# Optimization experiments

Hardware: AMD Instinct MI355X
Metric: run time of the kernel (lower is better)

## Reference

```python
import jax, jax.numpy as jnp
import numpy as np

B, T, E = 64, 512, 128
NODES, PATHS, OUT = 100000, 200000, 1000
PAD = 1  # padding_idx for node embedding


def setup_inputs() -> dict:
    key = jax.random.key(0)
    ks = jax.random.split(key, 10)
    starts = jax.random.randint(ks[0], (B, T), 0, NODES)
    paths = jax.random.randint(ks[1], (B, T), 0, PATHS)
    ends = jax.random.randint(ks[2], (B, T), 0, NODES)
    length = jax.random.randint(ks[3], (B,), 0, T)
    node_emb = jax.random.normal(ks[4], (NODES, E), dtype=jnp.float32)
    path_emb = jax.random.normal(ks[5], (PATHS, E), dtype=jnp.float32)
    W = jax.random.normal(ks[6], (E, 3 * E), dtype=jnp.float32)
    a = jax.random.normal(ks[7], (E,), dtype=jnp.float32)
    out_W = jax.random.normal(ks[8], (OUT, E), dtype=jnp.float32) * (1.0 / np.sqrt(E))
    out_b = jax.random.normal(ks[9], (OUT,), dtype=jnp.float32) * 0.01
    return dict(starts=starts, paths=paths, ends=ends, length=length,
                node_emb=node_emb, path_emb=path_emb, W=W, a=a,
                out_W=out_W, out_b=out_b)


def reference(starts, paths, ends, length, node_emb, path_emb, W, a, out_W, out_b):
    # padding_idx=1 -> that embedding row is zero
    node_emb = node_emb.at[PAD].set(0.0)
    es = node_emb[starts]          # [B,T,E]
    ep = path_emb[paths]           # [B,T,E]
    ee = node_emb[ends]            # [B,T,E]
    c = jnp.concatenate([es, ep, ee], axis=2)          # [B,T,3E]
    # dropout is identity in eval mode
    x = jnp.tanh(jnp.einsum('ed,btd->bte', W, c))      # [B,T,E]
    z = jax.nn.softmax(x @ a, axis=1)                  # [B,T] softmax over full T
    # original code sums only first length[i] attention weights (no renorm)
    mask = (jnp.arange(T)[None, :] < length[:, None]).astype(x.dtype)  # [B,T]
    v = jnp.einsum('bte,bt->be', x, z * mask)          # [B,E]
    return v @ out_W.T + out_b                          # [B,OUT]
```

## Files before the change

### kernel.cpp

```cpp
#include <hip/hip_runtime.h>

#define BB     64
#define TT     512
#define EE     128
#define NROWS  (BB * TT)
#define PADIDX 1
#define OUTN   1000

typedef __attribute__((ext_vector_type(8)))  short short8;
typedef __attribute__((ext_vector_type(16))) float f32x16;

__device__ __forceinline__ float tanh_fast(float v) {
    return 1.0f - 2.0f / (__expf(2.0f * v) + 1.0f);
}

__device__ __forceinline__ void split8(float4 a0, float4 a1, short8& hi, short8& lo) {
    float f[8] = {a0.x, a0.y, a0.z, a0.w, a1.x, a1.y, a1.z, a1.w};
#pragma unroll
    for (int i = 0; i < 8; ++i) {
        unsigned u = __float_as_uint(f[i]);
        unsigned r = (u + (0x7fffu + ((u >> 16) & 1u))) & 0xffff0000u;
        hi[i] = (short)(r >> 16);
        lo[i] = (short)(__float_as_uint(f[i] - __uint_as_float(r)) >> 16);
    }
}

__global__ __launch_bounds__(256)
void k_prep(const float* __restrict__ W, unsigned short* __restrict__ Whg,
            unsigned short* __restrict__ Wlg)
{
    const int id = blockIdx.x * 256 + threadIdx.x;
    const int j  = id & 7;
    const int l  = (id >> 3) & 63;
    const int r2 = id >> 9;
    const int ks = r2 % 24;
    const int et = r2 / 24;
    const int e  = et * 32 + (l & 31);
    const int k  = ks * 16 + (l >> 5) * 8 + j;

    const float v = W[e * 384 + k];
    unsigned u = __float_as_uint(v);
    unsigned r = (u + (0x7fffu + ((u >> 16) & 1u))) & 0xffff0000u;
    Whg[id] = (unsigned short)(r >> 16);
    Wlg[id] = (unsigned short)(__float_as_uint(v - __uint_as_float(r)) >> 16);
}

__global__ __launch_bounds__(256, 2)
void k_gemm_x(const int* __restrict__ starts, const int* __restrict__ paths,
              const int* __restrict__ ends,
              const float* __restrict__ node_emb, const float* __restrict__ path_emb,
              const unsigned short* __restrict__ Whg, const unsigned short* __restrict__ Wlg,
              const float* __restrict__ a, float* __restrict__ x, float* __restrict__ s)
{
    __shared__ float mrg[64 * 128];

    const int tid  = threadIdx.x;
    const int lane = tid & 63;
    const int w    = tid >> 6;
    const int mg   = w >> 1;
    const int kg   = w & 1;
    const int fr   = lane & 31;
    const int kh   = lane >> 5;
    const int r0   = blockIdx.x * 64;

    const int row = r0 + mg * 32 + fr;
    const int i0 = starts[row], i1 = paths[row], i2 = ends[row];
    const char* baseA0 = (const char*)node_emb + (size_t)i0 * 512 + kh * 32;
    const char* baseA1 = (const char*)path_emb + (size_t)i1 * 512 + kh * 32;
    const char* baseA2 = (const char*)node_emb + (size_t)i2 * 512 + kh * 32;
    const bool pad0 = (i0 == PADIDX), pad2 = (i2 == PADIDX);

    const char* pbh = (const char*)Whg + lane * 16;
    const char* pbl = (const char*)Wlg + lane * 16;

    f32x16 acc[4];
#pragma unroll
    for (int ni = 0; ni < 4; ++ni)
#pragma unroll
        for (int i = 0; i < 16; ++i) acc[ni][i] = 0.0f;

    float4 a0b[2], a1b[2];
    short8 bhb[2][4], blb[2][4];

#define ISSUE_A(SLOT, KS) do {                                                  \
    const int seg_ = (KS) >> 3;                                                 \
    const char* p_ = (seg_ == 0 ? baseA0 : (seg_ == 1 ? baseA1 : baseA2))       \
                   + ((KS) & 7) * 64;                                           \
    a0b[SLOT] = *(const float4*)p_;                                             \
    a1b[SLOT] = *(const float4*)(p_ + 16);                                      \
} while (0)

#define ISSUE_B(SLOT, KS) do {                                                  \
    _Pragma("unroll")                                                           \
    for (int ni_ = 0; ni_ < 4; ++ni_) {                                         \
        bhb[SLOT][ni_] = *(const short8*)(pbh + ni_ * 24576 + (KS) * 1024);     \
        blb[SLOT][ni_] = *(const short8*)(pbl + ni_ * 24576 + (KS) * 1024);     \
    }                                                                           \
} while (0)

#define KLOOP(KS0) do {                                                         \
    ISSUE_A(0, (KS0));  ISSUE_A(1, (KS0) + 1);  ISSUE_B(0, (KS0));              \
    _Pragma("unroll")                                                           \
    for (int j = 0; j < 12; ++j) {                                              \
        const int seg_c = ((KS0) + j) >> 3;                                     \
        float4 ca0 = a0b[j & 1], ca1 = a1b[j & 1];                              \
        const bool pad_ = (seg_c == 0) ? pad0 : ((seg_c == 2) ? pad2 : false);  \
        if (pad_) { ca0 = make_float4(0.f, 0.f, 0.f, 0.f); ca1 = ca0; }         \
        if (j + 2 < 12) ISSUE_A(j & 1, (KS0) + j + 2);                          \
        if (j + 1 < 12) ISSUE_B((j + 1) & 1, (KS0) + j + 1);                    \
        short8 ah, al;                                                          \
        split8(ca0, ca1, ah, al);                                               \
        _Pragma("unroll")                                                       \
        for (int ni = 0; ni < 4; ++ni) {                                        \
            acc[ni] = __builtin_amdgcn_mfma_f32_32x32x16_bf16(ah, bhb[j & 1][ni], acc[ni], 0, 0, 0); \
            acc[ni] = __builtin_amdgcn_mfma_f32_32x32x16_bf16(ah, blb[j & 1][ni], acc[ni], 0, 0, 0); \
            acc[ni] = __builtin_amdgcn_mfma_f32_32x32x16_bf16(al, bhb[j & 1][ni], acc[ni], 0, 0, 0); \
        }                                                                       \
    }                                                                           \
} while (0)

    if (kg == 0) KLOOP(0); else KLOOP(12);

#undef ISSUE_A
#undef ISSUE_B
#undef KLOOP

    if (kg == 1) {
#pragma unroll
        for (int ni = 0; ni < 4; ++ni)
#pragma unroll
            for (int r = 0; r < 16; ++r)
                mrg[(ni * 16 + r) * 128 + mg * 64 + lane] = acc[ni][r];
    }
    __syncthreads();

    if (kg == 0) {
#pragma unroll
        for (int ni = 0; ni < 4; ++ni)
#pragma unroll
            for (int r = 0; r < 16; ++r)
                acc[ni][r] += mrg[(ni * 16 + r) * 128 + mg * 64 + lane];

        float av[4];
#pragma unroll
        for (int ni = 0; ni < 4; ++ni) av[ni] = a[ni * 32 + fr];

        float sp[16];
#pragma unroll
        for (int r = 0; r < 16; ++r) sp[r] = 0.0f;

#pragma unroll
        for (int ni = 0; ni < 4; ++ni)
#pragma unroll
            for (int r = 0; r < 16; ++r) {
                const int rowl = (r & 3) + 8 * (r >> 2) + 4 * kh;
                const float tv = tanh_fast(acc[ni][r]);
                x[(size_t)(r0 + mg * 32 + rowl) * EE + ni * 32 + fr] = tv;
                sp[r] = fmaf(tv, av[ni], sp[r]);
            }

#pragma unroll
        for (int m = 1; m < 32; m <<= 1)
#pragma unroll
            for (int r = 0; r < 16; ++r) sp[r] += __shfl_xor(sp[r], m, 64);

        if (fr == 0) {
#pragma unroll
            for (int r = 0; r < 16; ++r) {
                const int rowl = (r & 3) + 8 * (r >> 2) + 4 * kh;
                s[r0 + mg * 32 + rowl] = sp[r];
            }
        }
    }
}

__global__ __launch_bounds__(256)
void k_attn(const float* __restrict__ s, const int* __restrict__ length,
            const float* __restrict__ x, float* __restrict__ v)
{
    __shared__ float sw[TT];
    __shared__ float red[256];

    const int b   = blockIdx.x >> 2;
    const int ec  = blockIdx.x & 3;
    const int tid = threadIdx.x;

    const float s0 = s[b * TT + tid];
    const float s1 = s[b * TT + 256 + tid];

    red[tid] = fmaxf(s0, s1);
    __syncthreads();
    for (int st = 128; st > 0; st >>= 1) {
        if (tid < st) red[tid] = fmaxf(red[tid], red[tid + st]);
        __syncthreads();
    }
    const float mx = red[0];
    __syncthreads();

    const float e0 = __expf(s0 - mx);
    const float e1 = __expf(s1 - mx);
    red[tid] = e0 + e1;
    __syncthreads();
    for (int st = 128; st > 0; st >>= 1) {
        if (tid < st) red[tid] += red[tid + st];
        __syncthreads();
    }
    const float inv = 1.0f / red[0];
    const int   len = length[b];
    __syncthreads();

    sw[tid]       = e0 * inv;
    sw[tid + 256] = e1 * inv;
    __syncthreads();

    const int e  = ec * 32 + (tid & 31);
    const int tp = tid >> 5;
    const float* xb = x + (size_t)b * TT * EE;
    float acc = 0.0f;
    for (int t = tp; t < len; t += 8)
        acc = fmaf(sw[t], xb[(size_t)t * EE + e], acc);

    red[tid] = acc;
    __syncthreads();
    if (tid < 32) {
        float r2 = 0.0f;
#pragma unroll
        for (int k = 0; k < 8; ++k) r2 += red[k * 32 + tid];
        v[b * EE + ec * 32 + tid] = r2;
    }
}

__global__ __launch_bounds__(256)
void k_out(const float* __restrict__ v, const float* __restrict__ out_W,
           const float* __restrict__ out_b, float* __restrict__ out)
{
    const int id = blockIdx.x * 256 + threadIdx.x;
    const int o  = id >> 6;
    const int bb = id & 63;

    const float4* vr = (const float4*)(v + bb * EE);
    const float4* wr = (const float4*)(out_W + o * EE);
    float acc = 0.0f;
#pragma unroll 8
    for (int qq = 0; qq < 32; ++qq) {
        const float4 a4 = vr[qq];
        const float4 b4 = wr[qq];
        acc = fmaf(a4.x, b4.x, acc);
        acc = fmaf(a4.y, b4.y, acc);
        acc = fmaf(a4.z, b4.z, acc);
        acc = fmaf(a4.w, b4.w, acc);
    }
    out[bb * OUTN + o] = acc + out_b[o];
}

extern "C" void kernel_launch(void* const* d_in, const int* in_sizes, int n_in,
                              void* d_out, int out_size, void* d_ws, size_t ws_size,
                              hipStream_t stream)
{
    const int*   starts   = (const int*)d_in[0];
    const int*   paths    = (const int*)d_in[1];
    const int*   ends     = (const int*)d_in[2];
    const int*   length   = (const int*)d_in[3];
    const float* node_emb = (const float*)d_in[4];
    const float* path_emb = (const float*)d_in[5];
    const float* W        = (const float*)d_in[6];
    const float* a        = (const float*)d_in[7];
    const float* out_W    = (const float*)d_in[8];
    const float* out_b    = (const float*)d_in[9];
    float*       out      = (float*)d_out;

    float* x = (float*)d_ws;
    float* s = x + (size_t)NROWS * EE;
    float* v = s + NROWS;
    unsigned short* Whg = (unsigned short*)(v + BB * EE);
    unsigned short* Wlg = Whg + 49152;

    k_prep<<<192, 256, 0, stream>>>(W, Whg, Wlg);
    k_gemm_x<<<NROWS / 64, 256, 0, stream>>>(starts, paths, ends,
                                             node_emb, path_emb, Whg, Wlg,
                                             a, x, s);
    k_attn<<<BB * 4, 256, 0, stream>>>(s, length, x, v);
    k_out<<<(BB * OUTN) / 256, 256, 0, stream>>>(v, out_W, out_b, out);
}
```

Before: 219.9 us.

## Fuse gemm, attention and output kernels into one persistent kernel with grid barriers

Result: slower. 330.6 us (+50.3%).

```diff
diff --git a/kernel.cpp b/kernel.cpp
--- a/kernel.cpp
+++ b/kernel.cpp
@@ -6,6 +6,7 @@
 #define NROWS  (BB * TT)
 #define PADIDX 1
 #define OUTN   1000
+#define NBLK   512
 
 typedef __attribute__((ext_vector_type(8)))  short short8;
 typedef __attribute__((ext_vector_type(16))) float f32x16;
@@ -46,13 +47,16 @@
 }
 
 __global__ __launch_bounds__(256, 2)
-void k_gemm_x(const int* __restrict__ starts, const int* __restrict__ paths,
-              const int* __restrict__ ends,
-              const float* __restrict__ node_emb, const float* __restrict__ path_emb,
-              const unsigned short* __restrict__ Whg, const unsigned short* __restrict__ Wlg,
-              const float* __restrict__ a, float* __restrict__ x, float* __restrict__ s)
+void k_fused(const int* __restrict__ starts, const int* __restrict__ paths,
+             const int* __restrict__ ends,  const int* __restrict__ length,
+             const float* __restrict__ node_emb, const float* __restrict__ path_emb,
+             const unsigned short* __restrict__ Whg, const unsigned short* __restrict__ Wlg,
+             const float* __restrict__ a, const float* __restrict__ out_W,
+             const float* __restrict__ out_b,
+             float* __restrict__ x, float* __restrict__ s, float* __restrict__ v,
+             float* __restrict__ out, unsigned* bar)
 {
-    __shared__ float mrg[64 * 128];
+    __shared__ float smem[64 * 128];
 
     const int tid  = threadIdx.x;
     const int lane = tid & 63;
@@ -63,24 +67,25 @@
     const int kh   = lane >> 5;
     const int r0   = blockIdx.x * 64;
 
-    const int row = r0 + mg * 32 + fr;
-    const int i0 = starts[row], i1 = paths[row], i2 = ends[row];
-    const char* baseA0 = (const char*)node_emb + (size_t)i0 * 512 + kh * 32;
-    const char* baseA1 = (const char*)path_emb + (size_t)i1 * 512 + kh * 32;
-    const char* baseA2 = (const char*)node_emb + (size_t)i2 * 512 + kh * 32;
-    const bool pad0 = (i0 == PADIDX), pad2 = (i2 == PADIDX);
-
-    const char* pbh = (const char*)Whg + lane * 16;
-    const char* pbl = (const char*)Wlg + lane * 16;
-
-    f32x16 acc[4];
-#pragma unroll
-    for (int ni = 0; ni < 4; ++ni)
-#pragma unroll
-        for (int i = 0; i < 16; ++i) acc[ni][i] = 0.0f;
-
-    float4 a0b[2], a1b[2];
-    short8 bhb[2][4], blb[2][4];
+    {
+        const int row = r0 + mg * 32 + fr;
+        const int i0 = starts[row], i1 = paths[row], i2 = ends[row];
+        const char* baseA0 = (const char*)node_emb + (size_t)i0 * 512 + kh * 32;
+        const char* baseA1 = (const char*)path_emb + (size_t)i1 * 512 + kh * 32;
+        const char* baseA2 = (const char*)node_emb + (size_t)i2 * 512 + kh * 32;
+        const bool pad0 = (i0 == PADIDX), pad2 = (i2 == PADIDX);
+
+        const char* pbh = (const char*)Whg + lane * 16;
+        const char* pbl = (const char*)Wlg + lane * 16;
+
+        f32x16 acc[4];
+#pragma unroll
+        for (int ni = 0; ni < 4; ++ni)
+#pragma unroll
+            for (int i = 0; i < 16; ++i) acc[ni][i] = 0.0f;
+
+        float4 a0b[2], a1b[2];
+        short8 bhb[2][4], blb[2][4];
 
 #define ISSUE_A(SLOT, KS) do {                                                  \
     const int seg_ = (KS) >> 3;                                                 \
@@ -119,138 +124,154 @@
     }                                                                           \
 } while (0)
 
-    if (kg == 0) KLOOP(0); else KLOOP(12);
+        if (kg == 0) KLOOP(0); else KLOOP(12);
 
 #undef ISSUE_A
 #undef ISSUE_B
 #undef KLOOP
 
-    if (kg == 1) {
-#pragma unroll
-        for (int ni = 0; ni < 4; ++ni)
-#pragma unroll
-            for (int r = 0; r < 16; ++r)
-                mrg[(ni * 16 + r) * 128 + mg * 64 + lane] = acc[ni][r];
-    }
+        if (kg == 1) {
+#pragma unroll
+            for (int ni = 0; ni < 4; ++ni)
+#pragma unroll
+                for (int r = 0; r < 16; ++r)
+                    smem[(ni * 16 + r) * 128 + mg * 64 + lane] = acc[ni][r];
+        }
+        __syncthreads();
+
+        if (kg == 0) {
+#pragma unroll
+            for (int ni = 0; ni < 4; ++ni)
+#pragma unroll
+                for (int r = 0; r < 16; ++r)
+                    acc[ni][r] += smem[(ni * 16 + r) * 128 + mg * 64 + lane];
+
+            float av[4];
+#pragma unroll
+            for (int ni = 0; ni < 4; ++ni) av[ni] = a[ni * 32 + fr];
+
+            float sp[16];
+#pragma unroll
+            for (int r = 0; r < 16; ++r) sp[r] = 0.0f;
+
+#pragma unroll
+            for (int ni = 0; ni < 4; ++ni)
+#pragma unroll
+                for (int r = 0; r < 16; ++r) {
+                    const int rowl = (r & 3) + 8 * (r >> 2) + 4 * kh;
+                    const float tv = tanh_fast(acc[ni][r]);
+                    x[(size_t)(r0 + mg * 32 + rowl) * EE + ni * 32 + fr] = tv;
+                    sp[r] = fmaf(tv, av[ni], sp[r]);
+                }
+
+#pragma unroll
+            for (int m = 1; m < 32; m <<= 1)
+#pragma unroll
+                for (int r = 0; r < 16; ++r) sp[r] += __shfl_xor(sp[r], m, 64);
+
+            if (fr == 0) {
+#pragma unroll
+                for (int r = 0; r < 16; ++r) {
+                    const int rowl = (r & 3) + 8 * (r >> 2) + 4 * kh;
+                    s[r0 + mg * 32 + rowl] = sp[r];
+                }
+            }
+        }
+    }
+
     __syncthreads();
-
-    if (kg == 0) {
-#pragma unroll
-        for (int ni = 0; ni < 4; ++ni)
-#pragma unroll
-            for (int r = 0; r < 16; ++r)
-                acc[ni][r] += mrg[(ni * 16 + r) * 128 + mg * 64 + lane];
-
-        float av[4];
-#pragma unroll
-        for (int ni = 0; ni < 4; ++ni) av[ni] = a[ni * 32 + fr];
-
-        float sp[16];
-#pragma unroll
-        for (int r = 0; r < 16; ++r) sp[r] = 0.0f;
-
-#pragma unroll
-        for (int ni = 0; ni < 4; ++ni)
-#pragma unroll
-            for (int r = 0; r < 16; ++r) {
-                const int rowl = (r & 3) + 8 * (r >> 2) + 4 * kh;
-                const float tv = tanh_fast(acc[ni][r]);
-                x[(size_t)(r0 + mg * 32 + rowl) * EE + ni * 32 + fr] = tv;
-                sp[r] = fmaf(tv, av[ni], sp[r]);
+    if (tid == 0) {
+        __threadfence();
+        atomicAdd(&bar[0], 1u);
+        while (__hip_atomic_load(&bar[0], __ATOMIC_RELAXED,
+                                 __HIP_MEMORY_SCOPE_AGENT) < NBLK)
+            __builtin_amdgcn_s_sleep(2);
+        __threadfence();
+    }
+    __syncthreads();
+
+    {
+        float* sw  = smem;
+        float* red = smem + TT;
+        const int b  = blockIdx.x >> 3;
+        const int ec = blockIdx.x & 7;
+
+        const float s0 = s[b * TT + tid];
+        const float s1 = s[b * TT + 256 + tid];
+
+        red[tid] = fmaxf(s0, s1);
+        __syncthreads();
+        for (int st = 128; st > 0; st >>= 1) {
+            if (tid < st) red[tid] = fmaxf(red[tid], red[tid + st]);
+            __syncthreads();
+        }
+        const float mx = red[0];
+        __syncthreads();
+
+        const float e0 = __expf(s0 - mx);
+        const float e1 = __expf(s1 - mx);
+        red[tid] = e0 + e1;
+        __syncthreads();
+        for (int st = 128; st > 0; st >>= 1) {
+            if (tid < st) red[tid] += red[tid + st];
+            __syncthreads();
+        }
+        const float inv = 1.0f / red[0];
+        const int   len = length[b];
+        __syncthreads();
+
+        sw[tid]       = e0 * inv;
+        sw[tid + 256] = e1 * inv;
+        __syncthreads();
+
+        const int e  = ec * 16 + (tid & 15);
+        const int tp = tid >> 4;
+        const float* xb = x + (size_t)b * TT * EE;
+        float acc2 = 0.0f;
+        for (int t = tp; t < len; t += 16)
+            acc2 = fmaf(sw[t], xb[(size_t)t * EE + e], acc2);
+
+        red[tid] = acc2;
+        __syncthreads();
+        if (tid < 16) {
+            float r2 = 0.0f;
+#pragma unroll
+            for (int k = 0; k < 16; ++k) r2 += red[k * 16 + tid];
+            v[b * EE + ec * 16 + tid] = r2;
+        }
+    }
+
+    __syncthreads();
+    if (tid == 0) {
+        __threadfence();
+        atomicAdd(&bar[1], 1u);
+        while (__hip_atomic_load(&bar[1], __ATOMIC_RELAXED,
+                                 __HIP_MEMORY_SCOPE_AGENT) < NBLK)
+            __builtin_amdgcn_s_sleep(2);
+        __threadfence();
+    }
+    __syncthreads();
+
+    {
+        const int id = blockIdx.x * 256 + tid;
+        if (id < BB * OUTN) {
+            const int o  = id >> 6;
+            const int bb = id & 63;
+            const float4* vr = (const float4*)(v + bb * EE);
+            const float4* wr = (const float4*)(out_W + o * EE);
+            float acc3 = 0.0f;
+#pragma unroll 8
+            for (int qq = 0; qq < 32; ++qq) {
+                const float4 a4 = vr[qq];
+                const float4 b4 = wr[qq];
+                acc3 = fmaf(a4.x, b4.x, acc3);
+                acc3 = fmaf(a4.y, b4.y, acc3);
+                acc3 = fmaf(a4.z, b4.z, acc3);
+                acc3 = fmaf(a4.w, b4.w, acc3);
             }
-
-#pragma unroll
-        for (int m = 1; m < 32; m <<= 1)
-#pragma unroll
-            for (int r = 0; r < 16; ++r) sp[r] += __shfl_xor(sp[r], m, 64);
-
-        if (fr == 0) {
-#pragma unroll
-            for (int r = 0; r < 16; ++r) {
-                const int rowl = (r & 3) + 8 * (r >> 2) + 4 * kh;
-                s[r0 + mg * 32 + rowl] = sp[r];
-            }
-        }
-    }
-}
-
-__global__ __launch_bounds__(256)
-void k_attn(const float* __restrict__ s, const int* __restrict__ length,
-            const float* __restrict__ x, float* __restrict__ v)
-{
-    __shared__ float sw[TT];
-    __shared__ float red[256];
-
-    const int b   = blockIdx.x >> 2;
-    const int ec  = blockIdx.x & 3;
-    const int tid = threadIdx.x;
-
-    const float s0 = s[b * TT + tid];
-    const float s1 = s[b * TT + 256 + tid];
-
-    red[tid] = fmaxf(s0, s1);
-    __syncthreads();
-    for (int st = 128; st > 0; st >>= 1) {
-        if (tid < st) red[tid] = fmaxf(red[tid], red[tid + st]);
-        __syncthreads();
-    }
-    const float mx = red[0];
-    __syncthreads();
-
-    const float e0 = __expf(s0 - mx);
-    const float e1 = __expf(s1 - mx);
-    red[tid] = e0 + e1;
-    __syncthreads();
-    for (int st = 128; st > 0; st >>= 1) {
-        if (tid < st) red[tid] += red[tid + st];
-        __syncthreads();
-    }
-    const float inv = 1.0f / red[0];
-    const int   len = length[b];
-    __syncthreads();
-
-    sw[tid]       = e0 * inv;
-    sw[tid + 256] = e1 * inv;
-    __syncthreads();
-
-    const int e  = ec * 32 + (tid & 31);
-    const int tp = tid >> 5;
-    const float* xb = x + (size_t)b * TT * EE;
-    float acc = 0.0f;
-    for (int t = tp; t < len; t += 8)
-        acc = fmaf(sw[t], xb[(size_t)t * EE + e], acc);
-
-    red[tid] = acc;
-    __syncthreads();
-    if (tid < 32) {
-        float r2 = 0.0f;
-#pragma unroll
-        for (int k = 0; k < 8; ++k) r2 += red[k * 32 + tid];
-        v[b * EE + ec * 32 + tid] = r2;
-    }
-}
-
-__global__ __launch_bounds__(256)
-void k_out(const float* __restrict__ v, const float* __restrict__ out_W,
-           const float* __restrict__ out_b, float* __restrict__ out)
-{
-    const int id = blockIdx.x * 256 + threadIdx.x;
-    const int o  = id >> 6;
-    const int bb = id & 63;
-
-    const float4* vr = (const float4*)(v + bb * EE);
-    const float4* wr = (const float4*)(out_W + o * EE);
-    float acc = 0.0f;
-#pragma unroll 8
-    for (int qq = 0; qq < 32; ++qq) {
-        const float4 a4 = vr[qq];
-        const float4 b4 = wr[qq];
-        acc = fmaf(a4.x, b4.x, acc);
-        acc = fmaf(a4.y, b4.y, acc);
-        acc = fmaf(a4.z, b4.z, acc);
-        acc = fmaf(a4.w, b4.w, acc);
-    }
-    out[bb * OUTN + o] = acc + out_b[o];
+            out[bb * OUTN + o] = acc3 + out_b[o];
+        }
+    }
 }
 
 extern "C" void kernel_launch(void* const* d_in, const int* in_sizes, int n_in,
@@ -274,11 +295,11 @@
     float* v = s + NROWS;
     unsigned short* Whg = (unsigned short*)(v + BB * EE);
     unsigned short* Wlg = Whg + 49152;
-
+    unsigned* bar = (unsigned*)(Wlg + 49152);
+
+    hipMemsetAsync(bar, 0, 16, stream);
     k_prep<<<192, 256, 0, stream>>>(W, Whg, Wlg);
-    k_gemm_x<<<NROWS / 64, 256, 0, stream>>>(starts, paths, ends,
-                                             node_emb, path_emb, Whg, Wlg,
-                                             a, x, s);
-    k_attn<<<BB * 4, 256, 0, stream>>>(s, length, x, v);
-    k_out<<<(BB * OUTN) / 256, 256, 0, stream>>>(v, out_W, out_b, out);
-}
+    k_fused<<<NBLK, 256, 0, stream>>>(starts, paths, ends, length,
+                                      node_emb, path_emb, Whg, Wlg,
+                                      a, out_W, out_b, x, s, v, out, bar);
+}
```
